# Kernel optimization log

Hardware: AMD Instinct MI355X
Metric: run time of the kernel (lower is better)

Reference implementation:

```python
import jax, jax.numpy as jnp
import numpy as np

D_MODEL = 1024
N_HEADS = 16
H_DIM = D_MODEL // N_HEADS
B, T = 2, 2048


def setup_inputs() -> dict:
    key = jax.random.key(0)
    ks = jax.random.split(key, 11)
    s = 1.0 / np.sqrt(D_MODEL)
    inp = {
        "q": jax.random.normal(ks[0], (B, T, D_MODEL), dtype=jnp.float32),
        "k": jax.random.normal(ks[1], (B, T, D_MODEL), dtype=jnp.float32),
        "v": jax.random.normal(ks[2], (B, T, D_MODEL), dtype=jnp.float32),
        "Wq": jax.random.normal(ks[3], (D_MODEL, D_MODEL), dtype=jnp.float32) * s,
        "bq": jnp.zeros((D_MODEL,), dtype=jnp.float32),
        "Wk": jax.random.normal(ks[4], (D_MODEL, D_MODEL), dtype=jnp.float32) * s,
        "bk": jnp.zeros((D_MODEL,), dtype=jnp.float32),
        "Wv": jax.random.normal(ks[5], (D_MODEL, D_MODEL), dtype=jnp.float32) * s,
        "bv": jnp.zeros((D_MODEL,), dtype=jnp.float32),
        "Wo": jax.random.normal(ks[6], (D_MODEL, D_MODEL), dtype=jnp.float32) * s,
        "bo": jnp.zeros((D_MODEL,), dtype=jnp.float32),
    }
    return inp


def reference(q, k, v, Wq, bq, Wk, bk, Wv, bv, Wo, bo):
    # Linear projections (W stored so that y = x @ W + b)
    qp = q @ Wq + bq  # [B,T,D]
    kp = k @ Wk + bk
    vp = v @ Wv + bv
    Bz, Tz, _ = qp.shape
    # [B,T,H,h] -> [B,H,T,h]
    qh = qp.reshape(Bz, Tz, N_HEADS, H_DIM).transpose(0, 2, 1, 3)
    kh = kp.reshape(Bz, Tz, N_HEADS, H_DIM).transpose(0, 2, 1, 3)
    vh = vp.reshape(Bz, Tz, N_HEADS, H_DIM).transpose(0, 2, 1, 3)
    scale = 1.0 / np.sqrt(H_DIM).astype(np.float32)
    scores = jnp.einsum('bhqd,bhkd->bhqk', qh, kh) * scale  # [B,H,T,T]
    attn = jax.nn.softmax(scores, axis=-1)  # dropout is identity in eval
    ctx = jnp.einsum('bhqk,bhkd->bhqd', attn, vh)  # [B,H,T,h]
    ctx = ctx.transpose(0, 2, 1, 3).reshape(Bz, Tz, D_MODEL)
    return ctx @ Wo + bo
```

## Files before the change

### kernel.cpp

```cpp
#include <hip/hip_runtime.h>

typedef __bf16 bf16x8 __attribute__((ext_vector_type(8)));
typedef float f32x4 __attribute__((ext_vector_type(4)));
typedef float f32x16 __attribute__((ext_vector_type(16)));
typedef unsigned short u16;
typedef unsigned short u16x8 __attribute__((ext_vector_type(8)));
typedef unsigned int u32;

#define MROWS 4096
#define DMODEL 1024
#define TSEQ 2048

__device__ __forceinline__ u32 bfr(float x) {
    u32 u = __float_as_uint(x);
    return (u + 0x7FFFu + ((u >> 16) & 1u)) >> 16;
}
__device__ __forceinline__ u32 pk2(float lo, float hi) { return bfr(lo) | (bfr(hi) << 16); }

__device__ __forceinline__ u32 cvtpk(float lo, float hi) {
    u32 r;
    asm("v_cvt_pk_bf16_f32 %0, %1, %2" : "=v"(r) : "v"(lo), "v"(hi));
    return r;
}

__device__ __forceinline__ void gl_lds16(const void* g, void* l) {
    __builtin_amdgcn_global_load_lds(
        (const __attribute__((address_space(1))) unsigned int*)g,
        (__attribute__((address_space(3))) unsigned int*)l, 16, 0, 0);
}

__global__ __launch_bounds__(256) void cvt_x(const float* __restrict__ q,
                                             const float* __restrict__ k,
                                             const float* __restrict__ v,
                                             u16* __restrict__ X) {
    int z = blockIdx.y;
    const float* src = (z == 0) ? q : (z == 1) ? k : v;
    size_t idx = ((size_t)blockIdx.x * 256 + threadIdx.x) * 8;
    const float4* s4 = (const float4*)(src + idx);
    float4 a = s4[0], b = s4[1];
    uint4 r;
    r.x = pk2(a.x, a.y); r.y = pk2(a.z, a.w);
    r.z = pk2(b.x, b.y); r.w = pk2(b.z, b.w);
    *(uint4*)(X + (size_t)z * 4194304 + idx) = r;
}

__global__ __launch_bounds__(256) void cvt_w(const float* __restrict__ w0,
                                             const float* __restrict__ w1,
                                             const float* __restrict__ w2,
                                             const float* __restrict__ w3,
                                             u16* __restrict__ Wt) {
    int z = blockIdx.z;
    const float* W = (z == 0) ? w0 : (z == 1) ? w1 : (z == 2) ? w2 : w3;
    u16* dst = Wt + (size_t)z * 1048576;
    __shared__ float tile[32][33];
    int n0 = blockIdx.x * 32, k0 = blockIdx.y * 32;
    int tx = threadIdx.x & 31, ty = threadIdx.x >> 5;
#pragma unroll
    for (int r = 0; r < 4; r++) {
        int row = ty + r * 8;
        tile[row][tx] = W[(size_t)(k0 + row) * DMODEL + n0 + tx];
    }
    __syncthreads();
#pragma unroll
    for (int r = 0; r < 4; r++) {
        int row = ty + r * 8;
        dst[(size_t)(n0 + row) * DMODEL + k0 + tx] = (u16)bfr(tile[tx][row]);
    }
}

template <int OUT_BF16>
__global__ __launch_bounds__(256) void gemm_bt(const u16* __restrict__ Abase,
                                               const u16* __restrict__ Btbase,
                                               const float* __restrict__ b0,
                                               const float* __restrict__ b1,
                                               const float* __restrict__ b2,
                                               void* __restrict__ Cout, int ldc) {
    int z = blockIdx.z;
    const u16* A  = Abase + (size_t)z * MROWS * DMODEL;
    const u16* Bt = Btbase + (size_t)z * DMODEL * DMODEL;
    const float* bias = (z == 0) ? b0 : (z == 1) ? b1 : b2;
    int id = blockIdx.y * 8 + blockIdx.x;
    int swz = (id & 7) * 32 + (id >> 3);
    int brow = (swz >> 3) * 128, bcol = (swz & 7) * 128;
    int t = threadIdx.x, lane = t & 63, wid = t >> 6;
    int wr = wid >> 1, wc = wid & 1;
    int lrow = lane & 15, g = lane >> 4;

    __shared__ __align__(16) u16 Asm[2][128 * 32];
    __shared__ __align__(16) u16 Bsm[2][128 * 32];

    f32x4 zero4 = {0.f, 0.f, 0.f, 0.f};
    f32x4 acc[4][4];
#pragma unroll
    for (int i = 0; i < 4; i++)
#pragma unroll
        for (int j = 0; j < 4; j++) acc[i][j] = zero4;

    auto stage = [&](int buf, int kt) {
        int k0 = kt * 32;
#pragma unroll
        for (int i = 0; i < 2; i++) {
            int c = i * 256 + wid * 64 + lane;
            int row = c >> 2, kc = c & 3;
            gl_lds16(A + (size_t)(brow + row) * DMODEL + k0 + kc * 8,
                     &Asm[buf][(i * 256 + wid * 64) * 8]);
            gl_lds16(Bt + (size_t)(bcol + row) * DMODEL + k0 + kc * 8,
                     &Bsm[buf][(i * 256 + wid * 64) * 8]);
        }
    };

    stage(0, 0);
    __syncthreads();
    for (int kt = 0; kt < 32; ++kt) {
        int cur = kt & 1;
        if (kt < 31) stage(cur ^ 1, kt + 1);
        bf16x8 af[4], bfv[4];
#pragma unroll
        for (int mi = 0; mi < 4; mi++)
            af[mi] = *(const bf16x8*)&Asm[cur][(wr * 64 + mi * 16 + lrow) * 32 + g * 8];
#pragma unroll
        for (int nj = 0; nj < 4; nj++)
            bfv[nj] = *(const bf16x8*)&Bsm[cur][(wc * 64 + nj * 16 + lrow) * 32 + g * 8];
#pragma unroll
        for (int mi = 0; mi < 4; mi++)
#pragma unroll
            for (int nj = 0; nj < 4; nj++)
                acc[mi][nj] = __builtin_amdgcn_mfma_f32_16x16x32_bf16(af[mi], bfv[nj], acc[mi][nj], 0, 0, 0);
        __syncthreads();
    }
#pragma unroll
    for (int nj = 0; nj < 4; nj++) {
        int n = bcol + wc * 64 + nj * 16 + lrow;
        float bv = bias[n];
#pragma unroll
        for (int mi = 0; mi < 4; mi++) {
#pragma unroll
            for (int r = 0; r < 4; r++) {
                int row = brow + wr * 64 + mi * 16 + g * 4 + r;
                float val = acc[mi][nj][r] + bv;
                if (OUT_BF16)
                    ((u16*)Cout)[(size_t)row * ldc + z * DMODEL + n] = (u16)bfr(val);
                else
                    ((float*)Cout)[(size_t)row * ldc + n] = val;
            }
        }
    }
}

__global__ __launch_bounds__(512, 1) void attn(const u16* __restrict__ QKV, u16* __restrict__ CTX) {
    int id = blockIdx.y * 8 + blockIdx.x;
    int swz = (id & 7) * 32 + (id >> 3);
    int qt = swz & 7;
    int bh = swz >> 3;
    int head = bh & 15;
    size_t base = (size_t)(bh >> 4) * TSEQ * 3072;
    int t = threadIdx.x;
    int tl = t & 255;
    int grp = t >> 8;
    int lane = t & 63, wid = t >> 6;
    int lw = wid & 3;
    int l31 = lane & 31, hf = lane >> 5;

    __shared__ __align__(16) u16 SH[32768];
    u16* Kg = SH + grp * 16384;
    u16* Vg = SH + grp * 16384 + 8192;

    int qwave = qt * 256 + lw * 64;
    const u16* QpA = QKV + base + (size_t)(qwave + l31) * 3072 + head * 64;
    const u16* QpB = QpA + 32 * 3072;
    bf16x8 qfA[4], qfB[4];
#pragma unroll
    for (int c = 0; c < 4; c++) {
        qfA[c] = *(const bf16x8*)(QpA + c * 16 + hf * 8);
        qfB[c] = *(const bf16x8*)(QpB + c * 16 + hf * 8);
    }

    f32x16 oA0 = {}, oA1 = {}, oB0 = {}, oB1 = {};
    float lA = 0.f, lB = 0.f;
    const float mC = 0.18033688f;

    int vkv = (tl & 31) * 2;
    int vd0 = (tl >> 5) * 8;
    int vslot = (vkv & ~12) | ((vkv & 4) << 1) | ((vkv & 8) >> 1);
    u16x8 vr0, vr1;

    auto stageK = [&](int buf, int kvb) {
#pragma unroll
        for (int i = 0; i < 2; i++) {
            int c = i * 256 + lw * 64 + lane;
            int kv = c >> 3, kc = (c & 7) ^ (kv & 7);
            gl_lds16(QKV + base + (size_t)(kvb * 64 + kv) * 3072 + 1024 + head * 64 + kc * 8,
                     &Kg[buf * 4096 + (i * 256 + lw * 64) * 8]);
        }
    };
    auto loadV = [&](int kvb) {
        const u16* Vp = QKV + base + (size_t)(kvb * 64) * 3072 + 2048 + head * 64;
        vr0 = *(const u16x8*)(Vp + (size_t)vkv * 3072 + vd0);
        vr1 = *(const u16x8*)(Vp + (size_t)(vkv + 1) * 3072 + vd0);
    };
    auto writeV = [&](int buf) {
#pragma unroll
        for (int e = 0; e < 8; e++) {
            int d = vd0 + e;
            int kvs = vslot ^ ((d >> 4) << 4) ^ ((d & 7) << 3);
            u32 p = (u32)vr0[e] | ((u32)vr1[e] << 16);
            *(u32*)&Vg[buf * 4096 + d * 64 + kvs] = p;
        }
    };

    int kvb0 = grp * 16;
    stageK(0, kvb0);
    loadV(kvb0);
    writeV(0);
    __syncthreads();

    int kx = (l31 & 7) * 8;

    for (int j = 0; j < 16; ++j) {
        int cur = j & 1, nxt = cur ^ 1;
        if (j < 15) { stageK(nxt, kvb0 + j + 1); loadV(kvb0 + j + 1); }

        f32x16 s0A = {}, s1A = {}, s0B = {}, s1B = {};
        const u16* kr0 = &Kg[cur * 4096 + l31 * 64];
        const u16* kr1 = kr0 + 32 * 64;
        __builtin_amdgcn_s_setprio(1);
#pragma unroll
        for (int c = 0; c < 4; c++) {
            int slot = ((2 * c + hf) * 8) ^ kx;
            bf16x8 a0 = *(const bf16x8*)(kr0 + slot);
            bf16x8 a1 = *(const bf16x8*)(kr1 + slot);
            s0A = __builtin_amdgcn_mfma_f32_32x32x16_bf16(a0, qfA[c], s0A, 0, 0, 0);
            s1A = __builtin_amdgcn_mfma_f32_32x32x16_bf16(a1, qfA[c], s1A, 0, 0, 0);
            s0B = __builtin_amdgcn_mfma_f32_32x32x16_bf16(a0, qfB[c], s0B, 0, 0, 0);
            s1B = __builtin_amdgcn_mfma_f32_32x32x16_bf16(a1, qfB[c], s1B, 0, 0, 0);
        }
        __builtin_amdgcn_s_setprio(0);

        float p0A[16], p1A[16], p0B[16], p1B[16];
#pragma unroll
        for (int r = 0; r < 16; r++) {
            p0A[r] = __builtin_amdgcn_exp2f(s0A[r] * mC);
            p1A[r] = __builtin_amdgcn_exp2f(s1A[r] * mC);
            p0B[r] = __builtin_amdgcn_exp2f(s0B[r] * mC);
            p1B[r] = __builtin_amdgcn_exp2f(s1B[r] * mC);
        }
        float sa = 0.f, sb = 0.f, sc = 0.f, sd = 0.f;
#pragma unroll
        for (int r = 0; r < 8; r++) {
            sa += p0A[r] + p0A[r + 8];
            sb += p1A[r] + p1A[r + 8];
            sc += p0B[r] + p0B[r + 8];
            sd += p1B[r] + p1B[r + 8];
        }
        lA += sa + sb;
        lB += sc + sd;

        union FragU { u32 u[4]; bf16x8 v; };
        bf16x8 paA[4], paB[4];
        {
            FragU fA, fB2, fC, fD;
#pragma unroll
            for (int w = 0; w < 4; w++) {
                fA.u[w]  = cvtpk(p0A[2 * w],     p0A[2 * w + 1]);
                fB2.u[w] = cvtpk(p0A[8 + 2 * w], p0A[9 + 2 * w]);
                fC.u[w]  = cvtpk(p1A[2 * w],     p1A[2 * w + 1]);
                fD.u[w]  = cvtpk(p1A[8 + 2 * w], p1A[9 + 2 * w]);
            }
            paA[0] = fA.v; paA[1] = fB2.v; paA[2] = fC.v; paA[3] = fD.v;
#pragma unroll
            for (int w = 0; w < 4; w++) {
                fA.u[w]  = cvtpk(p0B[2 * w],     p0B[2 * w + 1]);
                fB2.u[w] = cvtpk(p0B[8 + 2 * w], p0B[9 + 2 * w]);
                fC.u[w]  = cvtpk(p1B[2 * w],     p1B[2 * w + 1]);
                fD.u[w]  = cvtpk(p1B[8 + 2 * w], p1B[9 + 2 * w]);
            }
            paB[0] = fA.v; paB[1] = fB2.v; paB[2] = fC.v; paB[3] = fD.v;
        }

        if (j < 15) writeV(nxt);

        __builtin_amdgcn_s_setprio(1);
#pragma unroll
        for (int kc = 0; kc < 4; kc++) {
            int d0 = l31;
            int sl0 = ((2 * kc + hf) ^ (d0 & 7) ^ ((d0 >> 4) << 1)) * 8;
            bf16x8 v0 = *(const bf16x8*)&Vg[cur * 4096 + d0 * 64 + sl0];
            int d1 = 32 + l31;
            int sl1 = ((2 * kc + hf) ^ (d1 & 7) ^ ((d1 >> 4) << 1)) * 8;
            bf16x8 v1 = *(const bf16x8*)&Vg[cur * 4096 + d1 * 64 + sl1];
            oA0 = __builtin_amdgcn_mfma_f32_32x32x16_bf16(paA[kc], v0, oA0, 0, 0, 0);
            oA1 = __builtin_amdgcn_mfma_f32_32x32x16_bf16(paA[kc], v1, oA1, 0, 0, 0);
            oB0 = __builtin_amdgcn_mfma_f32_32x32x16_bf16(paB[kc], v0, oB0, 0, 0, 0);
            oB1 = __builtin_amdgcn_mfma_f32_32x32x16_bf16(paB[kc], v1, oB1, 0, 0, 0);
        }
        __builtin_amdgcn_s_setprio(0);
        __syncthreads();
    }

    lA += __shfl_xor(lA, 32);
    lB += __shfl_xor(lB, 32);

    float* FB = (float*)SH;
    if (grp == 1) {
#pragma unroll
        for (int r = 0; r < 16; r++) {
            FB[lw * 2048 + r * 64 + lane]        = oA0[r];
            FB[lw * 2048 + 1024 + r * 64 + lane] = oA1[r];
        }
        FB[8192 + lw * 64 + lane] = lA;
    }
    __syncthreads();
    if (grp == 0) {
        float l1 = FB[8192 + lw * 64 + lane];
        float rl = 1.0f / (lA + l1);
#pragma unroll
        for (int r = 0; r < 16; r++) {
            int qr = (r & 3) + 8 * (r >> 2) + 4 * hf;
            float rr = __shfl(rl, qr);
            float po0 = FB[lw * 2048 + r * 64 + lane];
            float po1 = FB[lw * 2048 + 1024 + r * 64 + lane];
            size_t rowoff = ((size_t)(bh >> 4) * TSEQ + qwave + qr) * DMODEL + head * 64;
            CTX[rowoff + l31]      = (u16)bfr((oA0[r] + po0) * rr);
            CTX[rowoff + 32 + l31] = (u16)bfr((oA1[r] + po1) * rr);
        }
    }
    __syncthreads();
    if (grp == 1) {
#pragma unroll
        for (int r = 0; r < 16; r++) {
            FB[lw * 2048 + r * 64 + lane]        = oB0[r];
            FB[lw * 2048 + 1024 + r * 64 + lane] = oB1[r];
        }
        FB[8192 + lw * 64 + lane] = lB;
    }
    __syncthreads();
    if (grp == 0) {
        float l1 = FB[8192 + lw * 64 + lane];
        float rl = 1.0f / (lB + l1);
#pragma unroll
        for (int r = 0; r < 16; r++) {
            int qr = (r & 3) + 8 * (r >> 2) + 4 * hf;
            float rr = __shfl(rl, qr);
            float po0 = FB[lw * 2048 + r * 64 + lane];
            float po1 = FB[lw * 2048 + 1024 + r * 64 + lane];
            size_t rowoff = ((size_t)(bh >> 4) * TSEQ + qwave + 32 + qr) * DMODEL + head * 64;
            CTX[rowoff + l31]      = (u16)bfr((oB0[r] + po0) * rr);
            CTX[rowoff + 32 + l31] = (u16)bfr((oB1[r] + po1) * rr);
        }
    }
}

extern "C" void kernel_launch(void* const* d_in, const int* in_sizes, int n_in,
                              void* d_out, int out_size, void* d_ws, size_t ws_size,
                              hipStream_t stream) {
    const float* q  = (const float*)d_in[0];
    const float* k  = (const float*)d_in[1];
    const float* v  = (const float*)d_in[2];
    const float* Wq = (const float*)d_in[3];
    const float* bq = (const float*)d_in[4];
    const float* Wk = (const float*)d_in[5];
    const float* bk = (const float*)d_in[6];
    const float* Wv = (const float*)d_in[7];
    const float* bv = (const float*)d_in[8];
    const float* Wo = (const float*)d_in[9];
    const float* bo = (const float*)d_in[10];

    char* ws = (char*)d_ws;
    u16* Xbf = (u16*)ws;
    u16* Wt  = (u16*)(ws + 25165824);
    u16* QKV = (u16*)(ws + 25165824 + 8388608);
    u16* CTX = Xbf;

    cvt_x<<<dim3(2048, 3), 256, 0, stream>>>(q, k, v, Xbf);
    cvt_w<<<dim3(32, 32, 4), 256, 0, stream>>>(Wq, Wk, Wv, Wo, Wt);
    gemm_bt<1><<<dim3(8, 32, 3), 256, 0, stream>>>(Xbf, Wt, bq, bk, bv, QKV, 3072);
    attn<<<dim3(8, 32), 512, 0, stream>>>(QKV, CTX);
    gemm_bt<0><<<dim3(8, 32, 1), 256, 0, stream>>>(CTX, Wt + 3 * 1048576, bo, bo, bo, d_out, 1024);
}
```

Baseline: 125.7 us.

## Use 4-stage LDS pipeline with XOR swizzle in projection GEMMs

The projection GEMM moves from a double-buffered LDS loop to a four-buffer ring that prefetches three k-chunks ahead. Each iteration waits with a partial vmcnt and a single barrier instead of a full sync. The global-to-LDS loads and the fragment reads use an XOR swizzle of the 16-byte chunk index, meant to reduce LDS bank conflicts, and s_setprio raises wave priority around the MFMA block. This targets load latency and barrier stalls in the GEMMs, at the cost of more LDS per block (64KB) and a correctness dependence on vmcnt counting matching the number of outstanding loads.

Measured after the change: 109.6 us. -12.9%, faster.

```diff
diff --git a/kernel.cpp b/kernel.cpp
--- a/kernel.cpp
+++ b/kernel.cpp
@@ -69,68 +69,82 @@
 }
 
 template <int OUT_BF16>
-__global__ __launch_bounds__(256) void gemm_bt(const u16* __restrict__ Abase,
-                                               const u16* __restrict__ Btbase,
-                                               const float* __restrict__ b0,
-                                               const float* __restrict__ b1,
-                                               const float* __restrict__ b2,
-                                               void* __restrict__ Cout, int ldc) {
+__global__ __launch_bounds__(256) void gemm4p(const u16* __restrict__ Abase,
+                                              const u16* __restrict__ Btbase,
+                                              const float* __restrict__ b0,
+                                              const float* __restrict__ b1,
+                                              const float* __restrict__ b2,
+                                              void* __restrict__ Cout, int ldc) {
     int z = blockIdx.z;
-    const u16* A  = Abase + (size_t)z * MROWS * DMODEL;
-    const u16* Bt = Btbase + (size_t)z * DMODEL * DMODEL;
+    const u16* A  = Abase + (size_t)z * 4194304;
+    const u16* Bt = Btbase + (size_t)z * 1048576;
     const float* bias = (z == 0) ? b0 : (z == 1) ? b1 : b2;
     int id = blockIdx.y * 8 + blockIdx.x;
     int swz = (id & 7) * 32 + (id >> 3);
     int brow = (swz >> 3) * 128, bcol = (swz & 7) * 128;
     int t = threadIdx.x, lane = t & 63, wid = t >> 6;
     int wr = wid >> 1, wc = wid & 1;
-    int lrow = lane & 15, g = lane >> 4;
-
-    __shared__ __align__(16) u16 Asm[2][128 * 32];
-    __shared__ __align__(16) u16 Bsm[2][128 * 32];
-
-    f32x4 zero4 = {0.f, 0.f, 0.f, 0.f};
+    int l15 = lane & 15, g = lane >> 4;
+    int sw = (l15 >> 1) & 3;
+
+    __shared__ __align__(16) u16 SH[32768];
+
     f32x4 acc[4][4];
 #pragma unroll
     for (int i = 0; i < 4; i++)
 #pragma unroll
-        for (int j = 0; j < 4; j++) acc[i][j] = zero4;
-
-    auto stage = [&](int buf, int kt) {
-        int k0 = kt * 32;
-#pragma unroll
-        for (int i = 0; i < 2; i++) {
-            int c = i * 256 + wid * 64 + lane;
-            int row = c >> 2, kc = c & 3;
-            gl_lds16(A + (size_t)(brow + row) * DMODEL + k0 + kc * 8,
-                     &Asm[buf][(i * 256 + wid * 64) * 8]);
-            gl_lds16(Bt + (size_t)(bcol + row) * DMODEL + k0 + kc * 8,
-                     &Bsm[buf][(i * 256 + wid * 64) * 8]);
-        }
-    };
-
-    stage(0, 0);
-    __syncthreads();
-    for (int kt = 0; kt < 32; ++kt) {
-        int cur = kt & 1;
-        if (kt < 31) stage(cur ^ 1, kt + 1);
+        for (int j = 0; j < 4; j++) acc[i][j] = f32x4{0.f, 0.f, 0.f, 0.f};
+
+    auto stage = [&](int kc) {
+        int b = kc & 3;
+#pragma unroll
+        for (int l = 0; l < 2; l++) {
+            int c = l * 256 + t;
+            int row = c >> 2, gch = c & 3;
+            int gs = gch ^ ((row >> 1) & 3);
+            gl_lds16(A + (size_t)(brow + row) * DMODEL + kc * 32 + gs * 8,
+                     &SH[b * 4096 + c * 8]);
+            gl_lds16(Bt + (size_t)(bcol + row) * DMODEL + kc * 32 + gs * 8,
+                     &SH[16384 + b * 4096 + c * 8]);
+        }
+    };
+
+    auto chunk_body = [&](int kc) {
+        const u16* Ab = &SH[(kc & 3) * 4096];
+        const u16* Bb = &SH[16384 + (kc & 3) * 4096];
         bf16x8 af[4], bfv[4];
 #pragma unroll
         for (int mi = 0; mi < 4; mi++)
-            af[mi] = *(const bf16x8*)&Asm[cur][(wr * 64 + mi * 16 + lrow) * 32 + g * 8];
+            af[mi] = *(const bf16x8*)&Ab[(wr * 64 + mi * 16 + l15) * 32 + ((g ^ sw) * 8)];
 #pragma unroll
         for (int nj = 0; nj < 4; nj++)
-            bfv[nj] = *(const bf16x8*)&Bsm[cur][(wc * 64 + nj * 16 + lrow) * 32 + g * 8];
+            bfv[nj] = *(const bf16x8*)&Bb[(wc * 64 + nj * 16 + l15) * 32 + ((g ^ sw) * 8)];
+        __builtin_amdgcn_s_setprio(1);
 #pragma unroll
         for (int mi = 0; mi < 4; mi++)
 #pragma unroll
             for (int nj = 0; nj < 4; nj++)
                 acc[mi][nj] = __builtin_amdgcn_mfma_f32_16x16x32_bf16(af[mi], bfv[nj], acc[mi][nj], 0, 0, 0);
-        __syncthreads();
-    }
+        __builtin_amdgcn_s_setprio(0);
+    };
+
+    stage(0); stage(1); stage(2);
+
+    for (int kc = 0; kc < 31; ++kc) {
+        asm volatile("s_waitcnt vmcnt(4)" ::: "memory");
+        __builtin_amdgcn_s_barrier();
+        __builtin_amdgcn_sched_barrier(0);
+        if (kc < 29) stage(kc + 3);
+        chunk_body(kc);
+    }
+    asm volatile("s_waitcnt vmcnt(0)" ::: "memory");
+    __builtin_amdgcn_s_barrier();
+    __builtin_amdgcn_sched_barrier(0);
+    chunk_body(31);
+
 #pragma unroll
     for (int nj = 0; nj < 4; nj++) {
-        int n = bcol + wc * 64 + nj * 16 + lrow;
+        int n = bcol + wc * 64 + nj * 16 + l15;
         float bv = bias[n];
 #pragma unroll
         for (int mi = 0; mi < 4; mi++) {
@@ -373,7 +387,7 @@
 
     cvt_x<<<dim3(2048, 3), 256, 0, stream>>>(q, k, v, Xbf);
     cvt_w<<<dim3(32, 32, 4), 256, 0, stream>>>(Wq, Wk, Wv, Wo, Wt);
-    gemm_bt<1><<<dim3(8, 32, 3), 256, 0, stream>>>(Xbf, Wt, bq, bk, bv, QKV, 3072);
+    gemm4p<1><<<dim3(8, 32, 3), 256, 0, stream>>>(Xbf, Wt, bq, bk, bv, QKV, 3072);
     attn<<<dim3(8, 32), 512, 0, stream>>>(QKV, CTX);
-    gemm_bt<0><<<dim3(8, 32, 1), 256, 0, stream>>>(CTX, Wt + 3 * 1048576, bo, bo, bo, d_out, 1024);
-}
+    gemm4p<0><<<dim3(8, 32, 1), 256, 0, stream>>>(CTX, Wt + 3 * 1048576, bo, bo, bo, d_out, 1024);
+}
```
